# Performance work log

Hardware: AMD Instinct MI355X
Metric: run time of the kernel (lower is better)

Reference implementation:

```python
import jax, jax.numpy as jnp
import numpy as np

N = 4096
RANK = 4
B = 2048
DT = 1.0
TAU = 1.0
ALPHA = float(np.sqrt(np.pi) / 2.0)  # erf slope so phi'(0)=1


def setup_inputs() -> dict:
    key = jax.random.key(0)
    k1, k2, k3, k4, k5, k6 = jax.random.split(key, 6)
    return {
        "x_t": jax.random.normal(k1, (1, B), dtype=jnp.float32),
        "h": jax.random.normal(k2, (N, B), dtype=jnp.float32),
        "m": jax.random.normal(k3, (N, 1), dtype=jnp.float32),
        "u": jax.random.normal(k4, (N, RANK), dtype=jnp.float32),
        "v": jax.random.normal(k5, (N, RANK), dtype=jnp.float32),
        "z": jax.random.normal(k6, (N, 1), dtype=jnp.float32),
    }


def reference(x_t, h, m, u, v, z):
    # phi(h) = erf(alpha * h)
    phi_h = jax.lax.erf(ALPHA * h)                      # [N, B]
    # W @ phi_h with W = (1/N) u v^T, reassociated to exploit low rank
    # (mathematically identical to materializing W)
    wph = (u @ (v.T @ phi_h)) / N                       # [N, B]
    h_update = wph + m @ x_t                            # [N, B]
    h_new = h + (DT / TAU) * (-h + h_update)            # [N, B]
    y = (z.T @ phi_h) / N                               # [1, B]
    return (y, h_new)
```

## Files before the change

kernel.cpp:

```cpp
#include <hip/hip_runtime.h>
#include <math.h>

#define N 4096
#define B 2048
#define RANK 4
#define ALPHA 0.8862269254527580f
#define INV_N (1.0f / 4096.0f)

#define RPB1 8
#define SPLITS (N / RPB1)
#define P (5 * B)
#define STRIPE 64
#define GRP 8
#define SPG (SPLITS / GRP)
#define RPB3 4

typedef float vf4 __attribute__((ext_vector_type(4)));
typedef unsigned short vus4 __attribute__((ext_vector_type(4)));

__device__ __forceinline__ float erf_fast(float t) {
  const float A = 0.140012288f;
  const float FP = 1.2732395447f;
  float t2 = t * t;
  float num = fmaf(A, t2, FP);
  float den = fmaf(A, t2, 1.0f);
  float r = t2 * num * __builtin_amdgcn_rcpf(den);
  float e = __expf(-r);
  float s = __builtin_amdgcn_sqrtf(fmaxf(1.0f - e, 0.0f));
  return copysignf(s, t);
}

__device__ __forceinline__ unsigned short f2bf(float f) {
  unsigned int u = __builtin_bit_cast(unsigned int, f);
  u += 0x7FFFu + ((u >> 16) & 1u);
  return (unsigned short)(u >> 16);
}
__device__ __forceinline__ float bf2f(unsigned short s) {
  unsigned int u = ((unsigned int)s) << 16;
  return __builtin_bit_cast(float, u);
}

__global__ __launch_bounds__(512) void k_reduce_partial(
    const float* __restrict__ h, const float* __restrict__ v,
    const float* __restrict__ z, unsigned short* __restrict__ partials) {
  const int tid = threadIdx.x;
  const int row0 = blockIdx.x * RPB1;

  vf4 a0 = {0.f, 0.f, 0.f, 0.f};
  vf4 a1 = a0, a2 = a0, a3 = a0, a4 = a0;

  const float* hp = h + (size_t)row0 * B + tid * 4;
#pragma unroll
  for (int r = 0; r < RPB1; ++r) {
    const vf4 hv = *(const vf4*)(hp + (size_t)r * B);
    vf4 p;
    p.x = erf_fast(ALPHA * hv.x);
    p.y = erf_fast(ALPHA * hv.y);
    p.z = erf_fast(ALPHA * hv.z);
    p.w = erf_fast(ALPHA * hv.w);
    const float v0 = v[(row0 + r) * RANK + 0];
    const float v1 = v[(row0 + r) * RANK + 1];
    const float v2 = v[(row0 + r) * RANK + 2];
    const float v3 = v[(row0 + r) * RANK + 3];
    const float zr = z[row0 + r];
    a0.x = fmaf(v0, p.x, a0.x); a0.y = fmaf(v0, p.y, a0.y);
    a0.z = fmaf(v0, p.z, a0.z); a0.w = fmaf(v0, p.w, a0.w);
    a1.x = fmaf(v1, p.x, a1.x); a1.y = fmaf(v1, p.y, a1.y);
    a1.z = fmaf(v1, p.z, a1.z); a1.w = fmaf(v1, p.w, a1.w);
    a2.x = fmaf(v2, p.x, a2.x); a2.y = fmaf(v2, p.y, a2.y);
    a2.z = fmaf(v2, p.z, a2.z); a2.w = fmaf(v2, p.w, a2.w);
    a3.x = fmaf(v3, p.x, a3.x); a3.y = fmaf(v3, p.y, a3.y);
    a3.z = fmaf(v3, p.z, a3.z); a3.w = fmaf(v3, p.w, a3.w);
    a4.x = fmaf(zr, p.x, a4.x); a4.y = fmaf(zr, p.y, a4.y);
    a4.z = fmaf(zr, p.z, a4.z); a4.w = fmaf(zr, p.w, a4.w);
  }

  unsigned short* pp = partials + (size_t)blockIdx.x * P + tid * 4;
  vus4 w0 = {f2bf(a0.x), f2bf(a0.y), f2bf(a0.z), f2bf(a0.w)};
  vus4 w1 = {f2bf(a1.x), f2bf(a1.y), f2bf(a1.z), f2bf(a1.w)};
  vus4 w2 = {f2bf(a2.x), f2bf(a2.y), f2bf(a2.z), f2bf(a2.w)};
  vus4 w3 = {f2bf(a3.x), f2bf(a3.y), f2bf(a3.z), f2bf(a3.w)};
  vus4 w4 = {f2bf(a4.x), f2bf(a4.y), f2bf(a4.z), f2bf(a4.w)};
  *(vus4*)(pp + 0 * B) = w0;
  *(vus4*)(pp + 1 * B) = w1;
  *(vus4*)(pp + 2 * B) = w2;
  *(vus4*)(pp + 3 * B) = w3;
  *(vus4*)(pp + 4 * B) = w4;
}

__global__ __launch_bounds__(512) void k_reduce_final(
    const unsigned short* __restrict__ partials, float* __restrict__ sfin,
    float* __restrict__ y) {
  __shared__ float red[GRP][STRIPE];
  const int c = threadIdx.x & (STRIPE - 1);
  const int g = threadIdx.x >> 6;
  const int f0 = blockIdx.x * STRIPE;
  const unsigned short* pp = partials + (size_t)(g * SPG) * P + f0 + c;
  float ssum = 0.f;
#pragma unroll 8
  for (int sp = 0; sp < SPG; ++sp)
    ssum += bf2f(pp[(size_t)sp * P]);
  red[g][c] = ssum;
  __syncthreads();
  if (threadIdx.x < STRIPE) {
    float tot = 0.f;
#pragma unroll
    for (int g2 = 0; g2 < GRP; ++g2)
      tot += red[g2][threadIdx.x];
    const int f = f0 + threadIdx.x;
    if (f < RANK * B)
      sfin[f] = tot;
    else
      y[f - RANK * B] = tot * INV_N;
  }
}

__global__ __launch_bounds__(256) void k_update(
    const float* __restrict__ sfin, const float* __restrict__ u,
    const float* __restrict__ m, const float* __restrict__ x,
    float* __restrict__ hnew) {
  const int tid = threadIdx.x;
  const int row0 = blockIdx.x * RPB3;
  const int c0 = tid * 4;

  const vf4 sA0 = *(const vf4*)(sfin + 0 * B + c0);
  const vf4 sA1 = *(const vf4*)(sfin + 1 * B + c0);
  const vf4 sA2 = *(const vf4*)(sfin + 2 * B + c0);
  const vf4 sA3 = *(const vf4*)(sfin + 3 * B + c0);
  const vf4 xa  = *(const vf4*)(x + c0);
  const vf4 sB0 = *(const vf4*)(sfin + 0 * B + c0 + 1024);
  const vf4 sB1 = *(const vf4*)(sfin + 1 * B + c0 + 1024);
  const vf4 sB2 = *(const vf4*)(sfin + 2 * B + c0 + 1024);
  const vf4 sB3 = *(const vf4*)(sfin + 3 * B + c0 + 1024);
  const vf4 xb  = *(const vf4*)(x + c0 + 1024);

  float* op = hnew + (size_t)row0 * B + c0;
#pragma unroll
  for (int i = 0; i < RPB3; ++i) {
    const int n = row0 + i;
    const vf4 uv = *(const vf4*)(u + (size_t)n * RANK);
    const float mv = m[n];
    vf4 oA, oB;
    oA.x = fmaf(mv, xa.x,
                (sA0.x * uv.x + sA1.x * uv.y + sA2.x * uv.z + sA3.x * uv.w) * INV_N);
    oA.y = fmaf(mv, xa.y,
                (sA0.y * uv.x + sA1.y * uv.y + sA2.y * uv.z + sA3.y * uv.w) * INV_N);
    oA.z = fmaf(mv, xa.z,
                (sA0.z * uv.x + sA1.z * uv.y + sA2.z * uv.z + sA3.z * uv.w) * INV_N);
    oA.w = fmaf(mv, xa.w,
                (sA0.w * uv.x + sA1.w * uv.y + sA2.w * uv.z + sA3.w * uv.w) * INV_N);
    oB.x = fmaf(mv, xb.x,
                (sB0.x * uv.x + sB1.x * uv.y + sB2.x * uv.z + sB3.x * uv.w) * INV_N);
    oB.y = fmaf(mv, xb.y,
                (sB0.y * uv.x + sB1.y * uv.y + sB2.y * uv.z + sB3.y * uv.w) * INV_N);
    oB.z = fmaf(mv, xb.z,
                (sB0.z * uv.x + sB1.z * uv.y + sB2.z * uv.z + sB3.z * uv.w) * INV_N);
    oB.w = fmaf(mv, xb.w,
                (sB0.w * uv.x + sB1.w * uv.y + sB2.w * uv.z + sB3.w * uv.w) * INV_N);
    __builtin_nontemporal_store(oA, (vf4*)(op + (size_t)i * B));
    __builtin_nontemporal_store(oB, (vf4*)(op + (size_t)i * B + 1024));
  }
}

extern "C" void kernel_launch(void* const* d_in, const int* in_sizes, int n_in,
                              void* d_out, int out_size, void* d_ws,
                              size_t ws_size, hipStream_t stream) {
  const float* x = (const float*)d_in[0];
  const float* h = (const float*)d_in[1];
  const float* m = (const float*)d_in[2];
  const float* u = (const float*)d_in[3];
  const float* v = (const float*)d_in[4];
  const float* z = (const float*)d_in[5];

  float* y = (float*)d_out;
  float* hnew = (float*)d_out + B;

  unsigned short* partials = (unsigned short*)d_ws;
  float* sfin = (float*)(partials + (size_t)SPLITS * P);

  k_reduce_partial<<<SPLITS, 512, 0, stream>>>(h, v, z, partials);
  k_reduce_final<<<P / STRIPE, 512, 0, stream>>>(partials, sfin, y);
  k_update<<<N / RPB3, 256, 0, stream>>>(sfin, u, m, x, hnew);
}
```

Before: 105.5 us.

## Replace two-stage bf16 partial reduction with float atomics into accumulator

The per-block partial sums are no longer written to a bf16 workspace and reduced in a separate kernel. Each block now adds its five rank/readout accumulators straight into a zeroed fp32 buffer with unsafeAtomicAdd, and the y output is written by the first block of the update kernel. This removes the partials round-trip and one kernel launch, at the cost of a memset and heavy atomic contention: 512 blocks each add to the same 10240 addresses. Summation order becomes nondeterministic.

```diff
diff --git a/kernel.cpp b/kernel.cpp
--- a/kernel.cpp
+++ b/kernel.cpp
@@ -8,15 +8,10 @@
 #define INV_N (1.0f / 4096.0f)
 
 #define RPB1 8
-#define SPLITS (N / RPB1)
-#define P (5 * B)
-#define STRIPE 64
-#define GRP 8
-#define SPG (SPLITS / GRP)
+#define BLOCKS1 (N / RPB1)
 #define RPB3 4
 
 typedef float vf4 __attribute__((ext_vector_type(4)));
-typedef unsigned short vus4 __attribute__((ext_vector_type(4)));
 
 __device__ __forceinline__ float erf_fast(float t) {
   const float A = 0.140012288f;
@@ -30,19 +25,9 @@
   return copysignf(s, t);
 }
 
-__device__ __forceinline__ unsigned short f2bf(float f) {
-  unsigned int u = __builtin_bit_cast(unsigned int, f);
-  u += 0x7FFFu + ((u >> 16) & 1u);
-  return (unsigned short)(u >> 16);
-}
-__device__ __forceinline__ float bf2f(unsigned short s) {
-  unsigned int u = ((unsigned int)s) << 16;
-  return __builtin_bit_cast(float, u);
-}
-
-__global__ __launch_bounds__(512) void k_reduce_partial(
+__global__ __launch_bounds__(512) void k_phi_reduce_atomic(
     const float* __restrict__ h, const float* __restrict__ v,
-    const float* __restrict__ z, unsigned short* __restrict__ partials) {
+    const float* __restrict__ z, float* __restrict__ sacc) {
   const int tid = threadIdx.x;
   const int row0 = blockIdx.x * RPB1;
 
@@ -75,50 +60,24 @@
     a4.z = fmaf(zr, p.z, a4.z); a4.w = fmaf(zr, p.w, a4.w);
   }
 
-  unsigned short* pp = partials + (size_t)blockIdx.x * P + tid * 4;
-  vus4 w0 = {f2bf(a0.x), f2bf(a0.y), f2bf(a0.z), f2bf(a0.w)};
-  vus4 w1 = {f2bf(a1.x), f2bf(a1.y), f2bf(a1.z), f2bf(a1.w)};
-  vus4 w2 = {f2bf(a2.x), f2bf(a2.y), f2bf(a2.z), f2bf(a2.w)};
-  vus4 w3 = {f2bf(a3.x), f2bf(a3.y), f2bf(a3.z), f2bf(a3.w)};
-  vus4 w4 = {f2bf(a4.x), f2bf(a4.y), f2bf(a4.z), f2bf(a4.w)};
-  *(vus4*)(pp + 0 * B) = w0;
-  *(vus4*)(pp + 1 * B) = w1;
-  *(vus4*)(pp + 2 * B) = w2;
-  *(vus4*)(pp + 3 * B) = w3;
-  *(vus4*)(pp + 4 * B) = w4;
-}
-
-__global__ __launch_bounds__(512) void k_reduce_final(
-    const unsigned short* __restrict__ partials, float* __restrict__ sfin,
-    float* __restrict__ y) {
-  __shared__ float red[GRP][STRIPE];
-  const int c = threadIdx.x & (STRIPE - 1);
-  const int g = threadIdx.x >> 6;
-  const int f0 = blockIdx.x * STRIPE;
-  const unsigned short* pp = partials + (size_t)(g * SPG) * P + f0 + c;
-  float ssum = 0.f;
-#pragma unroll 8
-  for (int sp = 0; sp < SPG; ++sp)
-    ssum += bf2f(pp[(size_t)sp * P]);
-  red[g][c] = ssum;
-  __syncthreads();
-  if (threadIdx.x < STRIPE) {
-    float tot = 0.f;
-#pragma unroll
-    for (int g2 = 0; g2 < GRP; ++g2)
-      tot += red[g2][threadIdx.x];
-    const int f = f0 + threadIdx.x;
-    if (f < RANK * B)
-      sfin[f] = tot;
-    else
-      y[f - RANK * B] = tot * INV_N;
-  }
+  float* sp = sacc + tid * 4;
+#define AADD(pl, acc)                        \
+  unsafeAtomicAdd(sp + (pl) * B + 0, acc.x); \
+  unsafeAtomicAdd(sp + (pl) * B + 1, acc.y); \
+  unsafeAtomicAdd(sp + (pl) * B + 2, acc.z); \
+  unsafeAtomicAdd(sp + (pl) * B + 3, acc.w);
+  AADD(0, a0)
+  AADD(1, a1)
+  AADD(2, a2)
+  AADD(3, a3)
+  AADD(4, a4)
+#undef AADD
 }
 
 __global__ __launch_bounds__(256) void k_update(
     const float* __restrict__ sfin, const float* __restrict__ u,
     const float* __restrict__ m, const float* __restrict__ x,
-    float* __restrict__ hnew) {
+    float* __restrict__ y, float* __restrict__ hnew) {
   const int tid = threadIdx.x;
   const int row0 = blockIdx.x * RPB3;
   const int c0 = tid * 4;
@@ -133,6 +92,15 @@
   const vf4 sB2 = *(const vf4*)(sfin + 2 * B + c0 + 1024);
   const vf4 sB3 = *(const vf4*)(sfin + 3 * B + c0 + 1024);
   const vf4 xb  = *(const vf4*)(x + c0 + 1024);
+
+  if (blockIdx.x == 0) {
+    vf4 ya = *(const vf4*)(sfin + 4 * B + c0);
+    vf4 yb = *(const vf4*)(sfin + 4 * B + c0 + 1024);
+    ya *= INV_N;
+    yb *= INV_N;
+    *(vf4*)(y + c0) = ya;
+    *(vf4*)(y + c0 + 1024) = yb;
+  }
 
   float* op = hnew + (size_t)row0 * B + c0;
 #pragma unroll
@@ -175,10 +143,9 @@
   float* y = (float*)d_out;
   float* hnew = (float*)d_out + B;
 
-  unsigned short* partials = (unsigned short*)d_ws;
-  float* sfin = (float*)(partials + (size_t)SPLITS * P);
+  float* sacc = (float*)d_ws;
 
-  k_reduce_partial<<<SPLITS, 512, 0, stream>>>(h, v, z, partials);
-  k_reduce_final<<<P / STRIPE, 512, 0, stream>>>(partials, sfin, y);
-  k_update<<<N / RPB3, 256, 0, stream>>>(sfin, u, m, x, hnew);
+  hipMemsetAsync(sacc, 0, (size_t)5 * B * sizeof(float), stream);
+  k_phi_reduce_atomic<<<BLOCKS1, 512, 0, stream>>>(h, v, z, sacc);
+  k_update<<<N / RPB3, 256, 0, stream>>>(sacc, u, m, x, y, hnew);
 }
```

Result: slower. 224.1 us (+112.4%).
